# Kernel optimization log

Measured on AMD Instinct MI355X. Metric: run time of the kernel, lower is better.

## Reference

```python
import jax, jax.numpy as jnp
import numpy as np
from jax import lax

B, L, D_IN, D_H = 4096, 64, 256, 200


def setup_inputs() -> dict:
    key = jax.random.key(0)
    ks = jax.random.split(key, 9)
    s_in = 1.0 / np.sqrt(D_IN)
    s_cv = 1.0 / np.sqrt(D_IN * 4)
    return {
        "x": jax.random.normal(ks[0], (B, L, D_IN), dtype=jnp.float32),
        "Wq": jax.random.uniform(ks[1], (D_H, D_IN), jnp.float32, -s_in, s_in),
        "bq": jax.random.uniform(ks[2], (D_H,), jnp.float32, -s_in, s_in),
        "Wk": jax.random.uniform(ks[3], (D_H, D_IN), jnp.float32, -s_in, s_in),
        "bk": jax.random.uniform(ks[4], (D_H,), jnp.float32, -s_in, s_in),
        "Wv": jax.random.uniform(ks[5], (D_H, D_IN), jnp.float32, -s_in, s_in),
        "bv": jax.random.uniform(ks[6], (D_H,), jnp.float32, -s_in, s_in),
        "conv_w": jax.random.uniform(ks[7], (D_H, D_IN, 4), jnp.float32, -s_cv, s_cv),
        "conv_b": jax.random.uniform(ks[8], (D_H,), jnp.float32, -s_cv, s_cv),
    }


def reference(x, Wq, bq, Wk, bk, Wv, bv, conv_w, conv_b):
    # x: [B, L=64, 256]
    q = jax.nn.relu(jnp.einsum("bld,hd->blh", x, Wq) + bq)  # [B,L,200]
    k = jax.nn.relu(jnp.einsum("bld,hd->blh", x, Wk) + bk)  # relu commutes with permute
    v = jax.nn.relu(jnp.einsum("bld,hd->blh", x, Wv) + bv)
    scores = jnp.einsum("blh,bmh->blm", q, k)               # bmm(q, k^T): [B,L,L]
    soft = jax.nn.softmax(scores, axis=1)                   # NOTE: dim=1 (over queries), as in original
    self_att = jnp.einsum("blm,bmh->blh", soft, v)          # [B,L,200]
    b = x.shape[0]
    self_att = self_att.reshape(b, -1, 4, 16).mean(axis=2).reshape(b, 16, -1)  # [B,16,200]
    word_att = x.reshape(b, 256, 64)                        # [B, C=256, len=64]
    conv = lax.conv_general_dilated(
        word_att, conv_w, window_strides=(4,), padding="VALID",
        dimension_numbers=("NCH", "OIH", "NCH"))            # [B,200,16]
    conv = conv + conv_b[None, :, None]
    conv = conv.reshape(b, 16, -1)                          # raw reshape, as in original
    return conv + self_att                                  # [B,16,200]
```

## Files before the change

### kernel.cpp

```cpp
#include <hip/hip_runtime.h>

typedef _Float16 f16x8 __attribute__((ext_vector_type(8)));
typedef _Float16 f16x4 __attribute__((ext_vector_type(4)));
typedef float f32x4 __attribute__((ext_vector_type(4)));

static __device__ __forceinline__ f32x4 MFMA(f16x8 a, f16x8 b, f32x4 c) {
  return __builtin_amdgcn_mfma_f32_16x16x32_f16(a, b, c, 0, 0, 0);
}

__global__ void wcvt(const float* __restrict__ Wq, const float* __restrict__ Wk,
                     const float* __restrict__ Wv, const float* __restrict__ cw,
                     const float* __restrict__ bq, const float* __restrict__ bk,
                     const float* __restrict__ bv,
                     _Float16* __restrict__ Wb,
                     _Float16* __restrict__ Wcb,
                     float* __restrict__ biasp) {
  int gt = blockIdx.x * blockDim.x + threadIdx.x;
  int gs = gridDim.x * blockDim.x;
  const int WN = 224 * 256;
  for (int i = gt; i < WN; i += gs) {
    int n = i >> 8;
    Wb[i]          = (n < 200) ? (_Float16)Wq[i] : (_Float16)0.f;
    Wb[WN + i]     = (n < 200) ? (_Float16)Wk[i] : (_Float16)0.f;
    Wb[2 * WN + i] = (n < 200) ? (_Float16)Wv[i] : (_Float16)0.f;
  }
  for (int i = gt; i < 224 * 1024; i += gs) {
    int o = i >> 10;
    Wcb[i] = (o < 200) ? (_Float16)cw[i] : (_Float16)0.f;
  }
  for (int i = gt; i < 224; i += gs) {
    biasp[i]       = (i < 200) ? bq[i] : 0.f;
    biasp[224 + i] = (i < 200) ? bk[i] : 0.f;
    biasp[448 + i] = (i < 200) ? bv[i] : 0.f;
  }
}

__global__ __launch_bounds__(512, 2) void k1_proj_conv(
    const float* __restrict__ x, const _Float16* __restrict__ Wb,
    const _Float16* __restrict__ Wcb, const float* __restrict__ biasp,
    const float* __restrict__ convb,
    _Float16* __restrict__ Qg, _Float16* __restrict__ Kg,
    _Float16* __restrict__ Vtg, float* __restrict__ out) {
  extern __shared__ char smem[];
  _Float16* Xl = (_Float16*)smem;
  const int tid = threadIdx.x, lane = tid & 63, wave = tid >> 6;
  const int li = lane & 15, g = lane >> 4;
  const int b0 = blockIdx.x * 4;

  const float* xb = x + (size_t)b0 * 16384;
#pragma unroll
  for (int j = 0; j < 32; j++) {
    int f = tid + 512 * j;
    float4 v = ((const float4*)xb)[f];
    int bt = f >> 12, rem = f & 4095, l = rem >> 6, c4 = rem & 63;
    f16x4 h;
    h.x = (_Float16)v.x; h.y = (_Float16)v.y;
    h.z = (_Float16)v.z; h.w = (_Float16)v.w;
    *(f16x4*)(Xl + bt * 16896 + l * 264 + c4 * 4) = h;
  }
  __syncthreads();

  for (int i = 0; i < 7; i++) {
    int u = wave + 8 * i;
    if (u < 42) {
      int p = u / 14, nt = u % 14, n = nt * 16 + li;
      const _Float16* wrow = Wb + p * 57344 + n * 256 + 8 * g;
      f16x8 bfr[8];
#pragma unroll
      for (int kk = 0; kk < 8; kk++) bfr[kk] = *(const f16x8*)(wrow + 32 * kk);
      float bias = biasp[p * 224 + n];
#pragma unroll
      for (int bt = 0; bt < 4; bt++) {
        const _Float16* xt = Xl + bt * 16896;
        f32x4 acc[4] = {};
#pragma unroll
        for (int kk = 0; kk < 8; kk++) {
#pragma unroll
          for (int mt = 0; mt < 4; mt++) {
            f16x8 af = *(const f16x8*)(xt + (mt * 16 + li) * 264 + 32 * kk + 8 * g);
            acc[mt] = MFMA(af, bfr[kk], acc[mt]);
          }
        }
        size_t bb = (size_t)(b0 + bt) * 14336;
#pragma unroll
        for (int mt = 0; mt < 4; mt++) {
#pragma unroll
          for (int r = 0; r < 4; r++) {
            int l = mt * 16 + 4 * g + r;
            float v = acc[mt][r] + bias;
            _Float16 hv = (_Float16)(v > 0.f ? v : 0.f);
            if (p == 0)      Qg[bb + l * 224 + n] = hv;
            else if (p == 1) Kg[bb + l * 224 + n] = hv;
            else             Vtg[bb + n * 64 + l] = hv;
          }
        }
      }
    } else {
      int nt = u - 42, o = nt * 16 + li;
      const _Float16* wrow = Wcb + o * 1024 + 8 * g;
      f32x4 acc[4] = {};
#pragma unroll 4
      for (int kk = 0; kk < 32; kk++) {
        f16x8 bf = *(const f16x8*)(wrow + 32 * kk);
        int i1 = kk * 8 + 2 * g;
        int i2 = i1 + 1;
#pragma unroll
        for (int bt = 0; bt < 4; bt++) {
          const _Float16* xt = Xl + bt * 16896;
          union { f16x4 h[2]; f16x8 v; } af;
          af.h[0] = *(const f16x4*)(xt + (i1 >> 2) * 264 + ((i1 & 3) << 6) + 4 * li);
          af.h[1] = *(const f16x4*)(xt + (i2 >> 2) * 264 + ((i2 & 3) << 6) + 4 * li);
          acc[bt] = MFMA(af.v, bf, acc[bt]);
        }
      }
      if (o < 200) {
        float cb = convb[o];
#pragma unroll
        for (int bt = 0; bt < 4; bt++) {
          float* ob = out + (size_t)(b0 + bt) * 3200 + o * 16;
#pragma unroll
          for (int r = 0; r < 4; r++) ob[4 * g + r] = acc[bt][r] + cb;
        }
      }
    }
  }
}

#define K3_LDS 68608
__global__ __launch_bounds__(256, 2) void k3_attn(
    const _Float16* __restrict__ Qg, const _Float16* __restrict__ Kg,
    const _Float16* __restrict__ Vtg, float* __restrict__ out) {
  extern __shared__ char smem[];
  _Float16* Qs = (_Float16*)smem;
  _Float16* Ks = (_Float16*)(smem + 29696);
  float*    Sf = (float*)smem;
  _Float16* Vt = (_Float16*)(smem + 29696);
  _Float16* Sb = (_Float16*)(smem + 59392);
  float*    Po = (float*)smem;

  const int b = blockIdx.x;
  const int tid = threadIdx.x, lane = tid & 63, wave = tid >> 6;
  const int li = lane & 15, g = lane >> 4;
  const size_t bb = (size_t)b * 14336;

#pragma unroll
  for (int i = 0; i < 7; i++) {
    int j = tid + 256 * i;
    f16x8 q = *(const f16x8*)(Qg + bb + j * 8);
    int row = j / 28, col = (j % 28) * 8;
    *(f16x8*)(Qs + row * 232 + col) = q;
  }
#pragma unroll
  for (int i = 0; i < 7; i++) {
    int j = tid + 256 * i;
    f16x8 k = *(const f16x8*)(Kg + bb + j * 8);
    int row = j / 28, col = (j % 28) * 8;
    *(f16x8*)(Ks + row * 232 + col) = k;
  }
  f16x8 vreg[7];
#pragma unroll
  for (int i = 0; i < 7; i++)
    vreg[i] = *(const f16x8*)(Vtg + bb + (tid + 256 * i) * 8);
  __syncthreads();

  f32x4 sacc[4] = {};
  {
    const int mt = wave;
#pragma unroll
    for (int kk = 0; kk < 7; kk++) {
      f16x8 qa = *(const f16x8*)(Qs + (mt * 16 + li) * 232 + kk * 32 + 8 * g);
#pragma unroll
      for (int nt = 0; nt < 4; nt++) {
        f16x8 kb = *(const f16x8*)(Ks + (nt * 16 + li) * 232 + kk * 32 + 8 * g);
        sacc[nt] = MFMA(qa, kb, sacc[nt]);
      }
    }
  }
  __syncthreads();

  {
    const int mt = wave;
#pragma unroll
    for (int nt = 0; nt < 4; nt++)
#pragma unroll
      for (int r = 0; r < 4; r++)
        Sf[(mt * 16 + 4 * g + r) * 65 + nt * 16 + li] = sacc[nt][r];
  }
#pragma unroll
  for (int i = 0; i < 7; i++) {
    int j = tid + 256 * i;
    int h = j >> 3, c = j & 7;
    *(f16x8*)(Vt + h * 64 + ((c ^ (h & 7)) << 3)) = vreg[i];
  }
  __syncthreads();

  {
    int m = tid >> 2, r4 = tid & 3;
    float vals[16], mx = -1e30f;
#pragma unroll
    for (int i2 = 0; i2 < 16; i2++) {
      float v = Sf[(r4 + 4 * i2) * 65 + m];
      vals[i2] = v; mx = fmaxf(mx, v);
    }
    mx = fmaxf(mx, __shfl_xor(mx, 1));
    mx = fmaxf(mx, __shfl_xor(mx, 2));
    float s = 0.f;
#pragma unroll
    for (int i2 = 0; i2 < 16; i2++) { vals[i2] = __expf(vals[i2] - mx); s += vals[i2]; }
    s += __shfl_xor(s, 1);
    s += __shfl_xor(s, 2);
    float inv = 1.f / s;
#pragma unroll
    for (int i2 = 0; i2 < 16; i2++)
      Sb[(r4 + 4 * i2) * 72 + m] = (_Float16)(vals[i2] * inv);
  }
  __syncthreads();

  for (int i = tid; i < 3400; i += 256) ((float*)smem)[i] = 0.f;
  __syncthreads();

  f16x8 pa[2][4];
#pragma unroll
  for (int kk = 0; kk < 2; kk++)
#pragma unroll
    for (int mt = 0; mt < 4; mt++)
      pa[kk][mt] = *(const f16x8*)(Sb + (mt * 16 + li) * 72 + kk * 32 + 8 * g);

  for (int ntl = wave; ntl < 14; ntl += 4) {
    int h = ntl * 16 + li;
    f16x8 vb[2];
#pragma unroll
    for (int kk = 0; kk < 2; kk++) {
      int cm = 4 * kk + g;
      vb[kk] = *(const f16x8*)(Vt + h * 64 + ((cm ^ (h & 7)) << 3));
    }
    f32x4 pacc[4] = {};
#pragma unroll
    for (int kk = 0; kk < 2; kk++)
#pragma unroll
      for (int mt = 0; mt < 4; mt++)
        pacc[mt] = MFMA(pa[kk][mt], vb[kk], pacc[mt]);
    if (h < 200) {
#pragma unroll
      for (int mt = 0; mt < 4; mt++)
#pragma unroll
        for (int r = 0; r < 4; r++) {
          int l = mt * 16 + 4 * g + r;
          int f = l * 200 + h;
          atomicAdd(&Po[(f >> 6) * 17 + (f & 15)], 0.25f * pacc[mt][r]);
        }
    }
  }
  __syncthreads();

  float* ob = out + (size_t)b * 3200;
  for (int t = tid; t < 3200; t += 256) {
    int c = t >> 4;
    ob[t] += Po[c * 17 + (t & 15)];
  }
}

#define FB_LDS 151296
__global__ __launch_bounds__(512, 2) void fused_fallback(
    const float* __restrict__ x, const _Float16* __restrict__ Wb,
    const _Float16* __restrict__ Wcb, const float* __restrict__ biasp,
    const float* __restrict__ convb, float* __restrict__ out) {
  extern __shared__ char smem[];
  _Float16* Xl = (_Float16*)smem;
  _Float16* Qs = (_Float16*)(smem + 33792);
  _Float16* Ks = (_Float16*)(smem + 63488);
  _Float16* Vt = (_Float16*)(smem + 93184);
  float* Sf    = (float*)(smem + 125440);
  _Float16* Sb = (_Float16*)(smem + 142080);
  float* SA    = (float*)(smem + 33792);
  float* Cv    = (float*)(smem + 125440);

  const int b = blockIdx.x;
  const int tid = threadIdx.x;
  const int lane = tid & 63;
  const int wave = tid >> 6;
  const int li = lane & 15;
  const int g = lane >> 4;

  const float* xb = x + (size_t)b * 16384;
  for (int i = tid; i < 4096; i += 512) {
    float4 v = ((const float4*)xb)[i];
    int e = i * 4;
    int l = e >> 8, d = e & 255;
    f16x4 h;
    h.x = (_Float16)v.x; h.y = (_Float16)v.y;
    h.z = (_Float16)v.z; h.w = (_Float16)v.w;
    *(f16x4*)(Xl + l * 264 + d) = h;
  }
  __syncthreads();

  for (int u = wave; u < 42; u += 8) {
    int p = u / 14, nt = u % 14;
    int n = nt * 16 + li;
    const _Float16* wrow = Wb + p * 57344 + n * 256 + 8 * g;
    f16x8 bfr[8];
#pragma unroll
    for (int kk = 0; kk < 8; kk++) bfr[kk] = *(const f16x8*)(wrow + kk * 32);
    float bias = biasp[p * 224 + n];
    for (int m = 0; m < 4; m++) {
      f32x4 acc = {0.f, 0.f, 0.f, 0.f};
      const _Float16* arow = Xl + (m * 16 + li) * 264 + 8 * g;
#pragma unroll
      for (int kk = 0; kk < 8; kk++) acc = MFMA(*(const f16x8*)(arow + kk * 32), bfr[kk], acc);
#pragma unroll
      for (int r = 0; r < 4; r++) {
        int row = m * 16 + 4 * g + r;
        float v = acc[r] + bias;
        v = v > 0.f ? v : 0.f;
        _Float16 hv = (_Float16)v;
        if (p == 0) Qs[row * 232 + n] = hv;
        else if (p == 1) Ks[row * 232 + n] = hv;
        else Vt[n * 72 + row] = hv;
      }
    }
  }
  __syncthreads();

  for (int t = wave * 2; t < wave * 2 + 2; t++) {
    int mt = t >> 2, nt = t & 3;
    f32x4 acc = {0.f, 0.f, 0.f, 0.f};
    const _Float16* qrow = Qs + (mt * 16 + li) * 232 + 8 * g;
    const _Float16* krow = Ks + (nt * 16 + li) * 232 + 8 * g;
#pragma unroll
    for (int kk = 0; kk < 7; kk++)
      acc = MFMA(*(const f16x8*)(qrow + kk * 32), *(const f16x8*)(krow + kk * 32), acc);
#pragma unroll
    for (int r = 0; r < 4; r++)
      Sf[(mt * 16 + 4 * g + r) * 65 + nt * 16 + li] = acc[r];
  }
  __syncthreads();

  {
    int m = tid >> 3, r = tid & 7;
    float vals[8];
    float mx = -1e30f;
#pragma unroll
    for (int i = 0; i < 8; i++) {
      float v = Sf[(r + 8 * i) * 65 + m];
      vals[i] = v;
      mx = fmaxf(mx, v);
    }
    mx = fmaxf(mx, __shfl_xor(mx, 1));
    mx = fmaxf(mx, __shfl_xor(mx, 2));
    mx = fmaxf(mx, __shfl_xor(mx, 4));
    float s = 0.f;
#pragma unroll
    for (int i = 0; i < 8; i++) { vals[i] = __expf(vals[i] - mx); s += vals[i]; }
    s += __shfl_xor(s, 1);
    s += __shfl_xor(s, 2);
    s += __shfl_xor(s, 4);
    float inv = 1.0f / s;
#pragma unroll
    for (int i = 0; i < 8; i++)
      Sb[(r + 8 * i) * 72 + m] = (_Float16)(vals[i] * inv);
  }
  __syncthreads();

  for (int nt = wave; nt < 14; nt += 8) {
    int o = nt * 16 + li;
    const _Float16* wrow = Wcb + o * 1024 + 8 * g;
    f32x4 acc = {0.f, 0.f, 0.f, 0.f};
#pragma unroll 4
    for (int kk = 0; kk < 32; kk++) {
      int i1 = kk * 8 + 2 * g;
      int i2 = i1 + 1;
      union { f16x4 h[2]; f16x8 v; } af;
      af.h[0] = *(const f16x4*)(Xl + (i1 >> 2) * 264 + ((i1 & 3) << 6) + 4 * li);
      af.h[1] = *(const f16x4*)(Xl + (i2 >> 2) * 264 + ((i2 & 3) << 6) + 4 * li);
      acc = MFMA(af.v, *(const f16x8*)(wrow + 32 * kk), acc);
    }
#pragma unroll
    for (int r = 0; r < 4; r++) Cv[(4 * g + r) * 226 + o] = acc[r];
  }

  for (int t = wave; t < 56; t += 8) {
    int mt = t / 14, nt = t % 14;
    f32x4 acc = {0.f, 0.f, 0.f, 0.f};
    const _Float16* arow = Sb + (mt * 16 + li) * 72 + 8 * g;
    const _Float16* brow = Vt + (nt * 16 + li) * 72 + 8 * g;
#pragma unroll
    for (int kk = 0; kk < 2; kk++)
      acc = MFMA(*(const f16x8*)(arow + kk * 32), *(const f16x8*)(brow + kk * 32), acc);
#pragma unroll
    for (int r = 0; r < 4; r++)
      SA[(mt * 16 + 4 * g + r) * 228 + (nt * 16 + li)] = acc[r];
  }
  __syncthreads();

  float* ob = out + (size_t)b * 3200;
  for (int t = tid; t < 3200; t += 512) {
    int c = t >> 4, s = t & 15;
    float cv = Cv[s * 226 + c] + convb[c];
    float pool = 0.f;
#pragma unroll
    for (int j = 0; j < 4; j++) {
      int flat = c * 64 + j * 16 + s;
      int l = flat / 200;
      int h = flat - l * 200;
      pool += SA[l * 228 + h];
    }
    ob[t] = cv + 0.25f * pool;
  }
}

extern "C" void kernel_launch(void* const* d_in, const int* in_sizes, int n_in,
                              void* d_out, int out_size, void* d_ws, size_t ws_size,
                              hipStream_t stream) {
  const float* x  = (const float*)d_in[0];
  const float* Wq = (const float*)d_in[1];
  const float* bq = (const float*)d_in[2];
  const float* Wk = (const float*)d_in[3];
  const float* bk = (const float*)d_in[4];
  const float* Wv = (const float*)d_in[5];
  const float* bv = (const float*)d_in[6];
  const float* cw = (const float*)d_in[7];
  const float* cb = (const float*)d_in[8];

  char* ws = (char*)d_ws;
  _Float16* Wb  = (_Float16*)ws;
  _Float16* Wcb = (_Float16*)(ws + 344064);
  float* biasp  = (float*)(ws + 802816);

  hipLaunchKernelGGL(wcvt, dim3(512), dim3(256), 0, stream,
                     Wq, Wk, Wv, cw, bq, bk, bv, Wb, Wcb, biasp);

  const size_t QKV_BASE = 805888ull;
  const size_t QKV_ONE  = 117440512ull;
  const size_t NEED = QKV_BASE + 3ull * QKV_ONE;

  if (ws_size >= NEED) {
    _Float16* Qg  = (_Float16*)(ws + QKV_BASE);
    _Float16* Kg  = (_Float16*)(ws + QKV_BASE + QKV_ONE);
    _Float16* Vtg = (_Float16*)(ws + QKV_BASE + 2 * QKV_ONE);

    hipFuncSetAttribute((const void*)k1_proj_conv,
                        hipFuncAttributeMaxDynamicSharedMemorySize, 135168);
    hipLaunchKernelGGL(k1_proj_conv, dim3(1024), dim3(512), 135168, stream,
                       x, Wb, Wcb, biasp, cb, Qg, Kg, Vtg, (float*)d_out);

    hipFuncSetAttribute((const void*)k3_attn,
                        hipFuncAttributeMaxDynamicSharedMemorySize, K3_LDS);
    hipLaunchKernelGGL(k3_attn, dim3(4096), dim3(256), K3_LDS, stream,
                       Qg, Kg, Vtg, (float*)d_out);
  } else {
    hipFuncSetAttribute((const void*)fused_fallback,
                        hipFuncAttributeMaxDynamicSharedMemorySize, FB_LDS);
    hipLaunchKernelGGL(fused_fallback, dim3(4096), dim3(512), FB_LDS, stream,
                       x, Wb, Wcb, biasp, cb, (float*)d_out);
  }
}
```

Before: 624.7 us.

## Halve k1 batch tile, swap MFMA operands for vectorized Q/K/V stores

Each k1 block now covers two batch elements instead of four, which halves LDS use and doubles the grid, and the launch bound requests four blocks per CU. The Q/K projection swaps the MFMA operand roles so the accumulator layout places four consecutive output features per lane, giving packed f16x4 stores instead of scattered scalar stores; V^T and the conv output are likewise written as vectors. Weight fragments are now reloaded per k-step rather than kept in registers across batch tiles, which trades more global weight reads for less register pressure.

```diff
diff --git a/kernel.cpp b/kernel.cpp
--- a/kernel.cpp
+++ b/kernel.cpp
@@ -35,7 +35,7 @@
   }
 }
 
-__global__ __launch_bounds__(512, 2) void k1_proj_conv(
+__global__ __launch_bounds__(512, 4) void k1_proj_conv(
     const float* __restrict__ x, const _Float16* __restrict__ Wb,
     const _Float16* __restrict__ Wcb, const float* __restrict__ biasp,
     const float* __restrict__ convb,
@@ -45,11 +45,11 @@
   _Float16* Xl = (_Float16*)smem;
   const int tid = threadIdx.x, lane = tid & 63, wave = tid >> 6;
   const int li = lane & 15, g = lane >> 4;
-  const int b0 = blockIdx.x * 4;
+  const int b0 = blockIdx.x * 2;
 
   const float* xb = x + (size_t)b0 * 16384;
 #pragma unroll
-  for (int j = 0; j < 32; j++) {
+  for (int j = 0; j < 16; j++) {
     int f = tid + 512 * j;
     float4 v = ((const float4*)xb)[f];
     int bt = f >> 12, rem = f & 4095, l = rem >> 6, c4 = rem & 63;
@@ -60,52 +60,82 @@
   }
   __syncthreads();
 
+#pragma unroll 1
   for (int i = 0; i < 7; i++) {
     int u = wave + 8 * i;
-    if (u < 42) {
-      int p = u / 14, nt = u % 14, n = nt * 16 + li;
-      const _Float16* wrow = Wb + p * 57344 + n * 256 + 8 * g;
-      f16x8 bfr[8];
-#pragma unroll
-      for (int kk = 0; kk < 8; kk++) bfr[kk] = *(const f16x8*)(wrow + 32 * kk);
-      float bias = biasp[p * 224 + n];
-#pragma unroll
-      for (int bt = 0; bt < 4; bt++) {
-        const _Float16* xt = Xl + bt * 16896;
-        f32x4 acc[4] = {};
-#pragma unroll
-        for (int kk = 0; kk < 8; kk++) {
+    if (u < 28) {
+      int p = u / 14, nt = u % 14;
+      const _Float16* wrow = Wb + p * 57344 + (nt * 16 + li) * 256 + 8 * g;
+      f32x4 acc[2][4] = {};
+#pragma unroll
+      for (int kk = 0; kk < 8; kk++) {
+        f16x8 aw = *(const f16x8*)(wrow + 32 * kk);
+#pragma unroll
+        for (int bt = 0; bt < 2; bt++)
 #pragma unroll
           for (int mt = 0; mt < 4; mt++) {
-            f16x8 af = *(const f16x8*)(xt + (mt * 16 + li) * 264 + 32 * kk + 8 * g);
-            acc[mt] = MFMA(af, bfr[kk], acc[mt]);
+            f16x8 bx = *(const f16x8*)(Xl + bt * 16896 + (mt * 16 + li) * 264 + 32 * kk + 8 * g);
+            acc[bt][mt] = MFMA(aw, bx, acc[bt][mt]);
           }
+      }
+      float4 b4 = *(const float4*)(biasp + p * 224 + nt * 16 + 4 * g);
+      _Float16* dst0 = (p == 0) ? Qg : Kg;
+#pragma unroll
+      for (int bt = 0; bt < 2; bt++) {
+        _Float16* db = dst0 + (size_t)(b0 + bt) * 14336;
+#pragma unroll
+        for (int mt = 0; mt < 4; mt++) {
+          f16x4 hv;
+          {
+            float v0 = acc[bt][mt][0] + b4.x; hv[0] = (_Float16)(v0 > 0.f ? v0 : 0.f);
+            float v1 = acc[bt][mt][1] + b4.y; hv[1] = (_Float16)(v1 > 0.f ? v1 : 0.f);
+            float v2 = acc[bt][mt][2] + b4.z; hv[2] = (_Float16)(v2 > 0.f ? v2 : 0.f);
+            float v3 = acc[bt][mt][3] + b4.w; hv[3] = (_Float16)(v3 > 0.f ? v3 : 0.f);
+          }
+          *(f16x4*)(db + (mt * 16 + li) * 224 + nt * 16 + 4 * g) = hv;
         }
-        size_t bb = (size_t)(b0 + bt) * 14336;
+      }
+    } else if (u < 42) {
+      int nt = u - 28;
+      const _Float16* wrow = Wb + 2 * 57344 + (nt * 16 + li) * 256 + 8 * g;
+      f32x4 acc[2][4] = {};
+#pragma unroll
+      for (int kk = 0; kk < 8; kk++) {
+        f16x8 bw = *(const f16x8*)(wrow + 32 * kk);
+#pragma unroll
+        for (int bt = 0; bt < 2; bt++)
+#pragma unroll
+          for (int mt = 0; mt < 4; mt++) {
+            f16x8 ax = *(const f16x8*)(Xl + bt * 16896 + (mt * 16 + li) * 264 + 32 * kk + 8 * g);
+            acc[bt][mt] = MFMA(ax, bw, acc[bt][mt]);
+          }
+      }
+      float bias = biasp[448 + nt * 16 + li];
+#pragma unroll
+      for (int bt = 0; bt < 2; bt++) {
+        _Float16* db = Vtg + (size_t)(b0 + bt) * 14336;
 #pragma unroll
         for (int mt = 0; mt < 4; mt++) {
+          f16x4 hv;
 #pragma unroll
           for (int r = 0; r < 4; r++) {
-            int l = mt * 16 + 4 * g + r;
-            float v = acc[mt][r] + bias;
-            _Float16 hv = (_Float16)(v > 0.f ? v : 0.f);
-            if (p == 0)      Qg[bb + l * 224 + n] = hv;
-            else if (p == 1) Kg[bb + l * 224 + n] = hv;
-            else             Vtg[bb + n * 64 + l] = hv;
+            float v = acc[bt][mt][r] + bias;
+            hv[r] = (_Float16)(v > 0.f ? v : 0.f);
           }
+          *(f16x4*)(db + (nt * 16 + li) * 64 + mt * 16 + 4 * g) = hv;
         }
       }
     } else {
       int nt = u - 42, o = nt * 16 + li;
       const _Float16* wrow = Wcb + o * 1024 + 8 * g;
-      f32x4 acc[4] = {};
+      f32x4 acc[2] = {};
 #pragma unroll 4
       for (int kk = 0; kk < 32; kk++) {
         f16x8 bf = *(const f16x8*)(wrow + 32 * kk);
         int i1 = kk * 8 + 2 * g;
         int i2 = i1 + 1;
 #pragma unroll
-        for (int bt = 0; bt < 4; bt++) {
+        for (int bt = 0; bt < 2; bt++) {
           const _Float16* xt = Xl + bt * 16896;
           union { f16x4 h[2]; f16x8 v; } af;
           af.h[0] = *(const f16x4*)(xt + (i1 >> 2) * 264 + ((i1 & 3) << 6) + 4 * li);
@@ -116,10 +146,11 @@
       if (o < 200) {
         float cb = convb[o];
 #pragma unroll
-        for (int bt = 0; bt < 4; bt++) {
-          float* ob = out + (size_t)(b0 + bt) * 3200 + o * 16;
-#pragma unroll
-          for (int r = 0; r < 4; r++) ob[4 * g + r] = acc[bt][r] + cb;
+        for (int bt = 0; bt < 2; bt++) {
+          float4 vo;
+          vo.x = acc[bt][0] + cb; vo.y = acc[bt][1] + cb;
+          vo.z = acc[bt][2] + cb; vo.w = acc[bt][3] + cb;
+          *(float4*)(out + (size_t)(b0 + bt) * 3200 + o * 16 + 4 * g) = vo;
         }
       }
     }
@@ -439,8 +470,8 @@
     _Float16* Vtg = (_Float16*)(ws + QKV_BASE + 2 * QKV_ONE);
 
     hipFuncSetAttribute((const void*)k1_proj_conv,
-                        hipFuncAttributeMaxDynamicSharedMemorySize, 135168);
-    hipLaunchKernelGGL(k1_proj_conv, dim3(1024), dim3(512), 135168, stream,
+                        hipFuncAttributeMaxDynamicSharedMemorySize, 67584);
+    hipLaunchKernelGGL(k1_proj_conv, dim3(2048), dim3(512), 67584, stream,
                        x, Wb, Wcb, biasp, cb, Qg, Kg, Vtg, (float*)d_out);
 
     hipFuncSetAttribute((const void*)k3_attn,
```

New measurement: 584.9 us. -6.4%, faster.
